# Performance work log

Measured on AMD Instinct MI355X. Metric: run time of the kernel, lower is better.

## Reference

```python
import jax, jax.numpy as jnp
import numpy as np

BS, N, H = 8, 64, 512
L = 5
HH, WW = 14, 14


def setup_inputs() -> dict:
    key = jax.random.key(0)
    ks = jax.random.split(key, 6)
    roi_feature_single = jax.random.normal(ks[0], (BS, N, H), dtype=jnp.float32)
    img_featmap = jax.random.normal(ks[1], (BS, H, HH, WW), dtype=jnp.float32)
    # torch init: weight ~ N(0, 0.01), bias = 0
    node_W = jax.random.normal(ks[2], (L, H, H), dtype=jnp.float32) * 0.01
    node_b = jnp.zeros((L, H), dtype=jnp.float32)
    edge_W = jax.random.normal(ks[3], (L, H, H), dtype=jnp.float32) * 0.01
    edge_b = jnp.zeros((L, H), dtype=jnp.float32)
    full_mask = jax.random.randint(ks[4], (BS, N, N), 0, 2, dtype=jnp.int32)
    return {
        "roi_feature_single": roi_feature_single,
        "img_featmap": img_featmap,
        "node_W": node_W,
        "node_b": node_b,
        "edge_W": edge_W,
        "edge_b": edge_b,
        "full_mask": full_mask,
    }


def reference(roi_feature_single, img_featmap, node_W, node_b, edge_W, edge_b, full_mask):
    # mask: [bs, N, N, 1], float
    mask = full_mask.astype(jnp.float32)[..., None]
    denom = jnp.sum(mask, axis=-2) + 1.0  # [bs, N, 1]

    # AdaptiveAvgPool2d((1,1)) on N*N repeats of img_featmap == global mean over (H, W)
    edge_init = jnp.mean(img_featmap, axis=(2, 3))  # [bs, hidden]
    edge_state = jnp.broadcast_to(edge_init[:, None, None, :], (BS, N, N, H))

    node_state = roi_feature_single  # [bs, N, hidden]

    for t in range(L):
        nm = jnp.einsum('bnh,oh->bno', node_state, node_W[t]) + node_b[t]          # node_fc
        em = jnp.einsum('bijh,oh->bijo', edge_state, edge_W[t]) + edge_b[t]        # edge_fc
        col = nm[:, None, :, :]                      # feature_col_large [bs,1,N,h]
        edge_feat = nm[:, :, None, :] + col + em     # row + col + edge messages
        edge_state = jax.nn.leaky_relu(edge_feat)    # negative_slope=0.01 (torch default)
        agg = jnp.sum(edge_state * col * mask, axis=-2)   # masked sum over j -> [bs,N,h]
        node_feat = (nm + agg) / denom
        node_state = node_state + jax.nn.leaky_relu(node_feat)

    roi_col = jnp.broadcast_to(node_state[:, :, None, :], (BS, N, N, H))
    roi_row = jnp.broadcast_to(node_state[:, None, :, :], (BS, N, N, H))
    return jnp.concatenate([roi_col, roi_row], axis=-1)  # [bs, N, N, 2*hidden]
```

## Files before the change

kernel.cpp:

```cpp
#include <hip/hip_runtime.h>
#include <hip/hip_bf16.h>

#define BS 8
#define NN 64
#define HD 512
#define NLAYER 5

typedef short bf16x8 __attribute__((ext_vector_type(8)));
typedef float f32x4 __attribute__((ext_vector_type(4)));

__device__ __forceinline__ float lrelu(float x) { return x > 0.f ? x : 0.01f * x; }

__device__ __forceinline__ void cp16(const void* g, void* l) {
    __builtin_amdgcn_global_load_lds(
        (const __attribute__((address_space(1))) unsigned int*)g,
        (__attribute__((address_space(3))) unsigned int*)l,
        16, 0, 0);
}

__global__ __launch_bounds__(256) void prep_kernel(
    const float* __restrict__ roi, const float* __restrict__ img,
    const float* __restrict__ nW, const float* __restrict__ eW,
    const int* __restrict__ mask,
    __hip_bfloat16* __restrict__ nWb, __hip_bfloat16* __restrict__ eWb,
    float* __restrict__ nodef, __hip_bfloat16* __restrict__ nodeb,
    float* __restrict__ edge_init, float* __restrict__ denom)
{
    int bid = blockIdx.x, tid = threadIdx.x;
    if (bid < 2560) {
        const float* src = (bid < 1280) ? nW : eW;
        __hip_bfloat16* dst = (bid < 1280) ? nWb : eWb;
        int base = ((bid < 1280) ? bid : bid - 1280) * 1024 + tid * 4;
#pragma unroll
        for (int k = 0; k < 4; ++k) dst[base + k] = __float2bfloat16(src[base + k]);
    } else if (bid < 2816) {
        int base = (bid - 2560) * 1024 + tid * 4;
#pragma unroll
        for (int k = 0; k < 4; ++k) {
            float v = roi[base + k];
            nodef[base + k] = v;
            nodeb[base + k] = __float2bfloat16(v);
        }
    } else if (bid < 3840) {
        int pid = (bid - 2816) * 4 + (tid >> 6);
        int l = tid & 63;
        const float* p = img + (size_t)pid * 196;
        float s = 0.f;
        for (int x = l; x < 196; x += 64) s += p[x];
#pragma unroll
        for (int off = 1; off < 64; off <<= 1) s += __shfl_xor(s, off, 64);
        if (l == 0) edge_init[pid] = s * (1.f / 196.f);
    } else {
        int pid = (bid - 3840) * 256 + tid;
        if (pid < 512) {
            const int* m = mask + pid * 64;
            int s = 0;
#pragma unroll
            for (int j = 0; j < 64; ++j) s += m[j];
            denom[pid] = (float)s + 1.f;
        }
    }
}

__global__ __launch_bounds__(256) void em0_kernel(
    const float* __restrict__ edge_init,
    const float* __restrict__ eW0,
    const float* __restrict__ eB0,
    float* __restrict__ em0)
{
    int W = blockIdx.x * 4 + (threadIdx.x >> 6);
    int l = threadIdx.x & 63;
    int b = W >> 9, o = W & 511;
    const float4* ei = (const float4*)(edge_init + b * 512);
    const float4* w4 = (const float4*)(eW0 + (size_t)o * 512);
    float4 a0 = ei[l * 2], a1 = ei[l * 2 + 1];
    float4 b0 = w4[l * 2], b1 = w4[l * 2 + 1];
    float s = a0.x * b0.x + a0.y * b0.y + a0.z * b0.z + a0.w * b0.w
            + a1.x * b1.x + a1.y * b1.y + a1.z * b1.z + a1.w * b1.w;
#pragma unroll
    for (int off = 1; off < 64; off <<= 1) s += __shfl_xor(s, off, 64);
    if (l == 0) em0[W] = s + eB0[o];
}

__global__ __launch_bounds__(256) void nm_gemm(
    const __hip_bfloat16* __restrict__ A,
    const __hip_bfloat16* __restrict__ W,
    const float* __restrict__ bias,
    float* __restrict__ nm)
{
    __shared__ __align__(16) __hip_bfloat16 sA[64 * 32];
    __shared__ __align__(16) __hip_bfloat16 sB[64 * 32];
    int tid = threadIdx.x;
    int bm = blockIdx.x, bn = blockIdx.y;
    int w = tid >> 6, l = tid & 63;
    int lq = l >> 4, lr = l & 15;

    const char* aBase = (const char*)A + (size_t)bm * 64 * 1024;
    const char* bBase = (const char*)W + (size_t)bn * 64 * 1024;
    int offG = (tid >> 2) * 1024 + (tid & 3) * 16;
    int offL = tid * 16;

    f32x4 acc[4] = {};

    for (int kt = 0; kt < 16; ++kt) {
        int ko = kt * 64;
        cp16(aBase + offG + ko, (char*)sA + offL);
        cp16(bBase + offG + ko, (char*)sB + offL);
        __syncthreads();
        bf16x8 af = *(const bf16x8*)&sA[(w * 16 + lr) * 32 + lq * 8];
#pragma unroll
        for (int ni = 0; ni < 4; ++ni) {
            bf16x8 bfv = *(const bf16x8*)&sB[(ni * 16 + lr) * 32 + lq * 8];
            acc[ni] = __builtin_amdgcn_mfma_f32_16x16x32_bf16(af, bfv, acc[ni], 0, 0, 0);
        }
        __syncthreads();
    }
#pragma unroll
    for (int ni = 0; ni < 4; ++ni) {
        int col = bn * 64 + ni * 16 + lr;
        float bv = bias[col];
#pragma unroll
        for (int r = 0; r < 4; ++r) {
            int row = bm * 64 + w * 16 + lq * 4 + r;
            nm[(size_t)row * 512 + col] = acc[ni][r] + bv;
        }
    }
}

__global__ __launch_bounds__(256) void edge_rank1(
    const float* __restrict__ nm, const float* __restrict__ em0,
    const int* __restrict__ mask,
    __hip_bfloat16* __restrict__ es_dst,
    const float* __restrict__ denom,
    float* __restrict__ nodef, __hip_bfloat16* __restrict__ nodeb)
{
    int g = blockIdx.x >> 1, ch = blockIdx.x & 1;
    int w = threadIdx.x >> 6, l = threadIdx.x & 63;
    int c = ch * 256 + w * 64 + l;
    int b = g >> 6;
    float nmi = nm[(size_t)g * 512 + c];
    float emb = em0[b * 512 + c];
    const float* nmb = nm + (size_t)b * 64 * 512;
    const int* mrow = mask + g * 64;
    __hip_bfloat16* erow = es_dst + (size_t)g * 64 * 512 + c;
    float aggv = 0.f;
#pragma unroll 4
    for (int j = 0; j < 64; ++j) {
        float nmj = nmb[j * 512 + c];
        float es = lrelu(nmi + nmj + emb);
        erow[(size_t)j * 512] = __float2bfloat16(es);
        aggv += es * nmj * (float)mrow[j];
    }
    float nf = (nmi + aggv) / denom[g];
    size_t idx = (size_t)g * 512 + c;
    float ns = nodef[idx] + lrelu(nf);
    nodef[idx] = ns;
    nodeb[idx] = __float2bfloat16(ns);
}

__global__ __launch_bounds__(256) void edge_fused(
    const __hip_bfloat16* __restrict__ es_src,
    const __hip_bfloat16* __restrict__ eW,
    const float* __restrict__ eB,
    const float* __restrict__ nm,
    const int* __restrict__ mask,
    __hip_bfloat16* __restrict__ es_dst,
    const float* __restrict__ denom,
    float* __restrict__ nodef, __hip_bfloat16* __restrict__ nodeb,
    int write_es)
{
    __shared__ __align__(16) __hip_bfloat16 sA[128 * 64];
    __shared__ __align__(16) __hip_bfloat16 sB[128 * 64];
    int tid = threadIdx.x;
    int bn = blockIdx.x, bm = blockIdx.y;
    int w = tid >> 6, l = tid & 63;
    int wm = w >> 1, wn = w & 1;
    int lq = l >> 4, lr = l & 15;

    const char* aBase = (const char*)es_src + (size_t)bm * 128 * 1024;
    const char* bBase = (const char*)eW + (size_t)bn * 128 * 1024;
    int gOff = (tid >> 3) * 1024 + (tid & 7) * 16;
    int lOff = tid * 16;

    f32x4 acc[4][4] = {};

    for (int kt = 0; kt < 8; ++kt) {
        int ko = kt * 128;
#pragma unroll
        for (int i = 0; i < 4; ++i) {
            cp16(aBase + gOff + i * 32768 + ko, (char*)sA + lOff + i * 4096);
            cp16(bBase + gOff + i * 32768 + ko, (char*)sB + lOff + i * 4096);
        }
        __syncthreads();
#pragma unroll
        for (int kk = 0; kk < 2; ++kk) {
            bf16x8 af[4], bfv[4];
#pragma unroll
            for (int mi = 0; mi < 4; ++mi)
                af[mi] = *(const bf16x8*)&sA[(wm * 64 + mi * 16 + lr) * 64 + kk * 32 + lq * 8];
#pragma unroll
            for (int ni = 0; ni < 4; ++ni)
                bfv[ni] = *(const bf16x8*)&sB[(wn * 64 + ni * 16 + lr) * 64 + kk * 32 + lq * 8];
#pragma unroll
            for (int mi = 0; mi < 4; ++mi)
#pragma unroll
                for (int ni = 0; ni < 4; ++ni)
                    acc[mi][ni] = __builtin_amdgcn_mfma_f32_16x16x32_bf16(af[mi], bfv[ni], acc[mi][ni], 0, 0, 0);
        }
        __syncthreads();
    }

    int g = bm * 2 + wm;
    int b = g >> 6;
    int cbase = bn * 128 + wn * 64;

    float nmraw[4], nmi[4];
#pragma unroll
    for (int ni = 0; ni < 4; ++ni) {
        int c = cbase + ni * 16 + lr;
        nmraw[ni] = nm[(size_t)g * 512 + c];
        nmi[ni] = nmraw[ni] + eB[c];
    }
    const float* nmb = nm + (size_t)b * 64 * 512;
    const int* mrow = mask + g * 64;
    float aggv[4] = {0.f, 0.f, 0.f, 0.f};

#pragma unroll
    for (int mi = 0; mi < 4; ++mi) {
#pragma unroll
        for (int r = 0; r < 4; ++r) {
            int j = mi * 16 + lq * 4 + r;
            float mf = (float)mrow[j];
            const float* nrow = nmb + (size_t)j * 512;
            size_t erow = ((size_t)(g * 64 + j)) * 512;
#pragma unroll
            for (int ni = 0; ni < 4; ++ni) {
                int c = cbase + ni * 16 + lr;
                float nmj = nrow[c];
                float es = lrelu(acc[mi][ni][r] + nmi[ni] + nmj);
                if (write_es) es_dst[erow + c] = __float2bfloat16(es);
                aggv[ni] += es * nmj * mf;
            }
        }
    }
    float dinv = denom[g];
#pragma unroll
    for (int ni = 0; ni < 4; ++ni) {
        float v = aggv[ni];
        v += __shfl_xor(v, 16, 64);
        v += __shfl_xor(v, 32, 64);
        if (lq == 0) {
            size_t idx = (size_t)g * 512 + cbase + ni * 16 + lr;
            float nf = (nmraw[ni] + v) / dinv;
            float ns = nodef[idx] + lrelu(nf);
            nodef[idx] = ns;
            nodeb[idx] = __float2bfloat16(ns);
        }
    }
}

__global__ __launch_bounds__(256) void out_kernel(
    const float* __restrict__ nodef, float* __restrict__ out)
{
    size_t ch = (size_t)blockIdx.x * 256 + threadIdx.x;
    int c4 = (int)(ch & 255);
    size_t r = ch >> 8;
    int b = (int)(r >> 12);
    int i = (int)((r >> 6) & 63);
    int j = (int)(r & 63);
    int c = c4 * 4;
    const float* src = (c < 512) ? (nodef + ((size_t)(b * 64 + i)) * 512 + c)
                                 : (nodef + ((size_t)(b * 64 + j)) * 512 + (c - 512));
    *reinterpret_cast<float4*>(out + ch * 4) = *reinterpret_cast<const float4*>(src);
}

extern "C" void kernel_launch(void* const* d_in, const int* in_sizes, int n_in,
                              void* d_out, int out_size, void* d_ws, size_t ws_size,
                              hipStream_t stream) {
    const float* roi  = (const float*)d_in[0];
    const float* img  = (const float*)d_in[1];
    const float* nW   = (const float*)d_in[2];
    const float* nB   = (const float*)d_in[3];
    const float* eW   = (const float*)d_in[4];
    const float* eB   = (const float*)d_in[5];
    const int*   mask = (const int*)d_in[6];

    char* ob = (char*)d_out;
    const size_t ES_BYTES = (size_t)32768 * 512 * 2;
    __hip_bfloat16* es0   = (__hip_bfloat16*)(ob);
    __hip_bfloat16* es1   = (__hip_bfloat16*)(ob + ES_BYTES);
    __hip_bfloat16* eWb   = (__hip_bfloat16*)(ob + 2 * ES_BYTES);
    __hip_bfloat16* nWb   = (__hip_bfloat16*)(ob + 2 * ES_BYTES + 2621440);
    __hip_bfloat16* nodeb = (__hip_bfloat16*)(ob + 2 * ES_BYTES + 5242880);
    float*          nm    = (float*)(ob + 2 * ES_BYTES + 5767168);
    float*       edge_init= (float*)(ob + 2 * ES_BYTES + 6815744);
    float*          em0   = (float*)(ob + 2 * ES_BYTES + 6832128);

    char* ws = (char*)d_ws;
    float* nodef = (float*)(ws);
    float* denom = (float*)(ws + 1048576);
    float* outp  = (float*)d_out;

    prep_kernel<<<3842, 256, 0, stream>>>(roi, img, nW, eW, mask,
                                          nWb, eWb, nodef, nodeb, edge_init, denom);
    em0_kernel<<<1024, 256, 0, stream>>>(edge_init, eW, eB, em0);

    nm_gemm<<<dim3(8, 8), 256, 0, stream>>>(nodeb, nWb, nB, nm);
    edge_rank1<<<1024, 256, 0, stream>>>(nm, em0, mask, es0, denom, nodef, nodeb);

    for (int t = 1; t < NLAYER; ++t) {
        const __hip_bfloat16* src = (t & 1) ? es0 : es1;
        __hip_bfloat16* dst       = (t & 1) ? es1 : es0;
        nm_gemm<<<dim3(8, 8), 256, 0, stream>>>(nodeb, nWb + (size_t)t * 262144,
                                                nB + t * 512, nm);
        edge_fused<<<dim3(4, 256), 256, 0, stream>>>(src, eWb + (size_t)t * 262144,
                                                     eB + t * 512, nm, mask,
                                                     dst, denom, nodef, nodeb,
                                                     (t < 4) ? 1 : 0);
    }

    out_kernel<<<32768, 256, 0, stream>>>(nodef, outp);
}
```

Measured before the change: 425.4 us.

## Fuse next-layer node GEMV into edge kernels and retile edge GEMM per node

Removes the separate nm_gemm launches by computing the next layer's node_fc as a per-row GEMV at the end of each edge kernel, using the freshly updated node state held in shared memory, with ping-pong nm buffers. The edge GEMM is retiled so that one block owns one node row (64 edges × all 512 outputs), which makes that fusion possible; the full weight slice is streamed from L2 by every block. The em0 matvec is merged with the first node GEMM, and the prep conversions are vectorized. The trade-off is more weight traffic per block, a serial fp32 GEMV tail and grids of only 512 blocks, in exchange for fewer launches and dependencies.

```diff
diff --git a/kernel.cpp b/kernel.cpp
--- a/kernel.cpp
+++ b/kernel.cpp
@@ -1,21 +1,24 @@
 #include <hip/hip_runtime.h>
 #include <hip/hip_bf16.h>
 
-#define BS 8
-#define NN 64
-#define HD 512
-#define NLAYER 5
 
 typedef short bf16x8 __attribute__((ext_vector_type(8)));
 typedef float f32x4 __attribute__((ext_vector_type(4)));
 
 __device__ __forceinline__ float lrelu(float x) { return x > 0.f ? x : 0.01f * x; }
+__device__ __forceinline__ float asf(unsigned int u) { return __uint_as_float(u); }
 
 __device__ __forceinline__ void cp16(const void* g, void* l) {
     __builtin_amdgcn_global_load_lds(
         (const __attribute__((address_space(1))) unsigned int*)g,
         (__attribute__((address_space(3))) unsigned int*)l,
         16, 0, 0);
+}
+
+__device__ __forceinline__ void cvt4store(__hip_bfloat16* dst, float4 v) {
+    __hip_bfloat16 tmp[4] = {__float2bfloat16(v.x), __float2bfloat16(v.y),
+                             __float2bfloat16(v.z), __float2bfloat16(v.w)};
+    *(uint2*)dst = *(const uint2*)tmp;
 }
 
 __global__ __launch_bounds__(256) void prep_kernel(
@@ -30,17 +33,13 @@
     if (bid < 2560) {
         const float* src = (bid < 1280) ? nW : eW;
         __hip_bfloat16* dst = (bid < 1280) ? nWb : eWb;
-        int base = ((bid < 1280) ? bid : bid - 1280) * 1024 + tid * 4;
-#pragma unroll
-        for (int k = 0; k < 4; ++k) dst[base + k] = __float2bfloat16(src[base + k]);
+        int i = ((bid < 1280) ? bid : bid - 1280) * 256 + tid;
+        cvt4store(dst + (size_t)i * 4, ((const float4*)src)[i]);
     } else if (bid < 2816) {
-        int base = (bid - 2560) * 1024 + tid * 4;
-#pragma unroll
-        for (int k = 0; k < 4; ++k) {
-            float v = roi[base + k];
-            nodef[base + k] = v;
-            nodeb[base + k] = __float2bfloat16(v);
-        }
+        int i = (bid - 2560) * 256 + tid;
+        float4 v = ((const float4*)roi)[i];
+        ((float4*)nodef)[i] = v;
+        cvt4store(nodeb + (size_t)i * 4, v);
     } else if (bid < 3840) {
         int pid = (bid - 2816) * 4 + (tid >> 6);
         int l = tid & 63;
@@ -48,7 +47,7 @@
         float s = 0.f;
         for (int x = l; x < 196; x += 64) s += p[x];
 #pragma unroll
-        for (int off = 1; off < 64; off <<= 1) s += __shfl_xor(s, off, 64);
+        for (int o = 1; o < 64; o <<= 1) s += __shfl_xor(s, o, 64);
         if (l == 0) edge_init[pid] = s * (1.f / 196.f);
     } else {
         int pid = (bid - 3840) * 256 + tid;
@@ -62,68 +61,86 @@
     }
 }
 
-__global__ __launch_bounds__(256) void em0_kernel(
-    const float* __restrict__ edge_init,
-    const float* __restrict__ eW0,
-    const float* __restrict__ eB0,
-    float* __restrict__ em0)
-{
-    int W = blockIdx.x * 4 + (threadIdx.x >> 6);
-    int l = threadIdx.x & 63;
-    int b = W >> 9, o = W & 511;
-    const float4* ei = (const float4*)(edge_init + b * 512);
-    const float4* w4 = (const float4*)(eW0 + (size_t)o * 512);
-    float4 a0 = ei[l * 2], a1 = ei[l * 2 + 1];
-    float4 b0 = w4[l * 2], b1 = w4[l * 2 + 1];
-    float s = a0.x * b0.x + a0.y * b0.y + a0.z * b0.z + a0.w * b0.w
-            + a1.x * b1.x + a1.y * b1.y + a1.z * b1.z + a1.w * b1.w;
-#pragma unroll
-    for (int off = 1; off < 64; off <<= 1) s += __shfl_xor(s, off, 64);
-    if (l == 0) em0[W] = s + eB0[o];
-}
-
-__global__ __launch_bounds__(256) void nm_gemm(
+__global__ __launch_bounds__(256) void nm0em0_kernel(
     const __hip_bfloat16* __restrict__ A,
-    const __hip_bfloat16* __restrict__ W,
-    const float* __restrict__ bias,
-    float* __restrict__ nm)
+    const __hip_bfloat16* __restrict__ W0,
+    const float* __restrict__ nB,
+    const float* __restrict__ edge_init, const float* __restrict__ eW,
+    const float* __restrict__ eB,
+    float* __restrict__ nm, float* __restrict__ em0)
 {
     __shared__ __align__(16) __hip_bfloat16 sA[64 * 32];
     __shared__ __align__(16) __hip_bfloat16 sB[64 * 32];
-    int tid = threadIdx.x;
-    int bm = blockIdx.x, bn = blockIdx.y;
-    int w = tid >> 6, l = tid & 63;
-    int lq = l >> 4, lr = l & 15;
-
-    const char* aBase = (const char*)A + (size_t)bm * 64 * 1024;
-    const char* bBase = (const char*)W + (size_t)bn * 64 * 1024;
-    int offG = (tid >> 2) * 1024 + (tid & 3) * 16;
-    int offL = tid * 16;
-
-    f32x4 acc[4] = {};
-
-    for (int kt = 0; kt < 16; ++kt) {
-        int ko = kt * 64;
-        cp16(aBase + offG + ko, (char*)sA + offL);
-        cp16(bBase + offG + ko, (char*)sB + offL);
-        __syncthreads();
-        bf16x8 af = *(const bf16x8*)&sA[(w * 16 + lr) * 32 + lq * 8];
+    int blk = blockIdx.x, tid = threadIdx.x;
+    int w = tid >> 6, l = tid & 63, lq = l >> 4, lr = l & 15;
+
+    if (blk < 64) {
+        int bm = blk >> 3, bn = blk & 7;
+        const char* aB = (const char*)A + (size_t)bm * 65536;
+        const char* bB = (const char*)W0 + (size_t)bn * 65536;
+        int offG = (tid >> 2) * 1024 + (tid & 3) * 16;
+        f32x4 acc[4] = {};
+        for (int kt = 0; kt < 16; ++kt) {
+            cp16(aB + offG + kt * 64, (char*)sA + tid * 16);
+            cp16(bB + offG + kt * 64, (char*)sB + tid * 16);
+            __syncthreads();
+            bf16x8 af = *(const bf16x8*)&sA[(w * 16 + lr) * 32 + lq * 8];
+#pragma unroll
+            for (int ni = 0; ni < 4; ++ni) {
+                bf16x8 bv = *(const bf16x8*)&sB[(ni * 16 + lr) * 32 + lq * 8];
+                acc[ni] = __builtin_amdgcn_mfma_f32_16x16x32_bf16(af, bv, acc[ni], 0, 0, 0);
+            }
+            __syncthreads();
+        }
 #pragma unroll
         for (int ni = 0; ni < 4; ++ni) {
-            bf16x8 bfv = *(const bf16x8*)&sB[(ni * 16 + lr) * 32 + lq * 8];
-            acc[ni] = __builtin_amdgcn_mfma_f32_16x16x32_bf16(af, bfv, acc[ni], 0, 0, 0);
-        }
-        __syncthreads();
-    }
-#pragma unroll
-    for (int ni = 0; ni < 4; ++ni) {
-        int col = bn * 64 + ni * 16 + lr;
-        float bv = bias[col];
-#pragma unroll
-        for (int r = 0; r < 4; ++r) {
-            int row = bm * 64 + w * 16 + lq * 4 + r;
-            nm[(size_t)row * 512 + col] = acc[ni][r] + bv;
-        }
+            int col = bn * 64 + ni * 16 + lr;
+            float bv = nB[col];
+#pragma unroll
+            for (int r = 0; r < 4; ++r) {
+                int row = bm * 64 + w * 16 + lq * 4 + r;
+                nm[(size_t)row * 512 + col] = acc[ni][r] + bv;
+            }
+        }
+    } else {
+        int wid = (blk - 64) * 4 + w;
+#pragma unroll
+        for (int k = 0; k < 8; ++k) {
+            int d = wid * 8 + k;
+            int b = d >> 9, o = d & 511;
+            const float4* ei = (const float4*)(edge_init + b * 512);
+            const float4* wv = (const float4*)(eW + (size_t)o * 512);
+            float4 a0 = ei[l * 2], a1 = ei[l * 2 + 1];
+            float4 b0 = wv[l * 2], b1 = wv[l * 2 + 1];
+            float s = a0.x * b0.x + a0.y * b0.y + a0.z * b0.z + a0.w * b0.w
+                    + a1.x * b1.x + a1.y * b1.y + a1.z * b1.z + a1.w * b1.w;
+#pragma unroll
+            for (int o2 = 1; o2 < 64; o2 <<= 1) s += __shfl_xor(s, o2, 64);
+            if (l == 0) em0[d] = s + eB[o];
+        }
+    }
+}
+
+__device__ __forceinline__ void gemv_next(
+    const float* snode, const __hip_bfloat16* __restrict__ Wn,
+    const float* __restrict__ bn, float* __restrict__ nm_out, int g, int tid)
+{
+    const float4* nr4 = (const float4*)snode;
+#pragma unroll
+    for (int oo = 0; oo < 2; ++oo) {
+        int o = tid + oo * 256;
+        const bf16x8* wr = (const bf16x8*)(Wn + (size_t)o * 512);
+        float s = 0.f;
+#pragma unroll 8
+        for (int k = 0; k < 64; ++k) {
+            union { bf16x8 v; uint4 u; } W; W.v = wr[k];
+            float4 n0 = nr4[2 * k], n1 = nr4[2 * k + 1];
+            s += asf(W.u.x << 16) * n0.x + asf(W.u.x & 0xFFFF0000u) * n0.y;
+            s += asf(W.u.y << 16) * n0.z + asf(W.u.y & 0xFFFF0000u) * n0.w;
+            s += asf(W.u.z << 16) * n1.x + asf(W.u.z & 0xFFFF0000u) * n1.y;
+            s += asf(W.u.w << 16) * n1.z + asf(W.u.w & 0xFFFF0000u) * n1.w;
+        }
+        nm_out[(size_t)g * 512 + o] = s + bn[o];
     }
 }
 
@@ -131,100 +148,98 @@
     const float* __restrict__ nm, const float* __restrict__ em0,
     const int* __restrict__ mask,
     __hip_bfloat16* __restrict__ es_dst,
-    const float* __restrict__ denom,
-    float* __restrict__ nodef, __hip_bfloat16* __restrict__ nodeb)
-{
-    int g = blockIdx.x >> 1, ch = blockIdx.x & 1;
-    int w = threadIdx.x >> 6, l = threadIdx.x & 63;
-    int c = ch * 256 + w * 64 + l;
-    int b = g >> 6;
-    float nmi = nm[(size_t)g * 512 + c];
-    float emb = em0[b * 512 + c];
-    const float* nmb = nm + (size_t)b * 64 * 512;
+    const float* __restrict__ denom, float* __restrict__ nodef,
+    const __hip_bfloat16* __restrict__ Wn, const float* __restrict__ bn,
+    float* __restrict__ nm_out)
+{
+    __shared__ float snode[512];
+    int g = blockIdx.x, tid = threadIdx.x, b = g >> 6;
+    const float* nmb = nm + (size_t)b * 32768;
     const int* mrow = mask + g * 64;
-    __hip_bfloat16* erow = es_dst + (size_t)g * 64 * 512 + c;
-    float aggv = 0.f;
+    float dv = denom[g];
+#pragma unroll
+    for (int cc = tid; cc < 512; cc += 256) {
+        float nmi = nm[(size_t)g * 512 + cc];
+        float emb = em0[b * 512 + cc];
+        __hip_bfloat16* erow = es_dst + (size_t)(g * 64) * 512 + cc;
+        float aggv = 0.f;
 #pragma unroll 4
-    for (int j = 0; j < 64; ++j) {
-        float nmj = nmb[j * 512 + c];
-        float es = lrelu(nmi + nmj + emb);
-        erow[(size_t)j * 512] = __float2bfloat16(es);
-        aggv += es * nmj * (float)mrow[j];
-    }
-    float nf = (nmi + aggv) / denom[g];
-    size_t idx = (size_t)g * 512 + c;
-    float ns = nodef[idx] + lrelu(nf);
-    nodef[idx] = ns;
-    nodeb[idx] = __float2bfloat16(ns);
-}
-
-__global__ __launch_bounds__(256) void edge_fused(
+        for (int j = 0; j < 64; ++j) {
+            float nmj = nmb[j * 512 + cc];
+            float es = lrelu(nmi + nmj + emb);
+            erow[(size_t)j * 512] = __float2bfloat16(es);
+            aggv += es * nmj * (float)mrow[j];
+        }
+        float nf = (nmi + aggv) / dv;
+        size_t idx = (size_t)g * 512 + cc;
+        float ns = nodef[idx] + lrelu(nf);
+        nodef[idx] = ns;
+        snode[cc] = ns;
+    }
+    __syncthreads();
+    gemv_next(snode, Wn, bn, nm_out, g, tid);
+}
+
+__global__ void __launch_bounds__(256, 2) edge_kernel(
     const __hip_bfloat16* __restrict__ es_src,
-    const __hip_bfloat16* __restrict__ eW,
-    const float* __restrict__ eB,
-    const float* __restrict__ nm,
+    const __hip_bfloat16* __restrict__ eWt,
+    const float* __restrict__ eBt,
+    const float* __restrict__ nm_in,
     const int* __restrict__ mask,
     __hip_bfloat16* __restrict__ es_dst,
-    const float* __restrict__ denom,
-    float* __restrict__ nodef, __hip_bfloat16* __restrict__ nodeb,
-    int write_es)
-{
-    __shared__ __align__(16) __hip_bfloat16 sA[128 * 64];
-    __shared__ __align__(16) __hip_bfloat16 sB[128 * 64];
-    int tid = threadIdx.x;
-    int bn = blockIdx.x, bm = blockIdx.y;
-    int w = tid >> 6, l = tid & 63;
-    int wm = w >> 1, wn = w & 1;
-    int lq = l >> 4, lr = l & 15;
-
-    const char* aBase = (const char*)es_src + (size_t)bm * 128 * 1024;
-    const char* bBase = (const char*)eW + (size_t)bn * 128 * 1024;
-    int gOff = (tid >> 3) * 1024 + (tid & 7) * 16;
-    int lOff = tid * 16;
-
-    f32x4 acc[4][4] = {};
-
-    for (int kt = 0; kt < 8; ++kt) {
-        int ko = kt * 128;
-#pragma unroll
-        for (int i = 0; i < 4; ++i) {
-            cp16(aBase + gOff + i * 32768 + ko, (char*)sA + lOff + i * 4096);
-            cp16(bBase + gOff + i * 32768 + ko, (char*)sB + lOff + i * 4096);
-        }
+    const float* __restrict__ denom, float* __restrict__ nodef,
+    const __hip_bfloat16* __restrict__ Wn, const float* __restrict__ bn,
+    float* __restrict__ nm_out,
+    int write_es, int do_gemv)
+{
+    __shared__ __align__(16) __hip_bfloat16 sh[18432];
+    __hip_bfloat16* sA = sh;
+    __hip_bfloat16* sB = sh + 2048;
+
+    int g = blockIdx.x, tid = threadIdx.x;
+    int w = tid >> 6, l = tid & 63, lq = l >> 4, lr = l & 15;
+    int b = g >> 6;
+
+    const char* aB = (const char*)es_src + (size_t)g * 65536;
+    const char* bB = (const char*)eWt;
+    int aOff = (tid >> 2) * 1024 + (tid & 3) * 16;
+
+    f32x4 acc[4][8] = {};
+    for (int kt = 0; kt < 16; ++kt) {
+        int ko = kt * 64;
+        cp16(aB + aOff + ko, (char*)sA + tid * 16);
+#pragma unroll
+        for (int i = 0; i < 8; ++i)
+            cp16(bB + aOff + i * 65536 + ko, (char*)sB + tid * 16 + i * 4096);
         __syncthreads();
-#pragma unroll
-        for (int kk = 0; kk < 2; ++kk) {
-            bf16x8 af[4], bfv[4];
-#pragma unroll
-            for (int mi = 0; mi < 4; ++mi)
-                af[mi] = *(const bf16x8*)&sA[(wm * 64 + mi * 16 + lr) * 64 + kk * 32 + lq * 8];
-#pragma unroll
-            for (int ni = 0; ni < 4; ++ni)
-                bfv[ni] = *(const bf16x8*)&sB[(wn * 64 + ni * 16 + lr) * 64 + kk * 32 + lq * 8];
-#pragma unroll
-            for (int mi = 0; mi < 4; ++mi)
-#pragma unroll
-                for (int ni = 0; ni < 4; ++ni)
-                    acc[mi][ni] = __builtin_amdgcn_mfma_f32_16x16x32_bf16(af[mi], bfv[ni], acc[mi][ni], 0, 0, 0);
-        }
+        bf16x8 af[4], bv[8];
+#pragma unroll
+        for (int mi = 0; mi < 4; ++mi)
+            af[mi] = *(const bf16x8*)&sA[(mi * 16 + lr) * 32 + lq * 8];
+#pragma unroll
+        for (int ni = 0; ni < 8; ++ni)
+            bv[ni] = *(const bf16x8*)&sB[(w * 128 + ni * 16 + lr) * 32 + lq * 8];
+#pragma unroll
+        for (int mi = 0; mi < 4; ++mi)
+#pragma unroll
+            for (int ni = 0; ni < 8; ++ni)
+                acc[mi][ni] = __builtin_amdgcn_mfma_f32_16x16x32_bf16(af[mi], bv[ni], acc[mi][ni], 0, 0, 0);
         __syncthreads();
     }
 
-    int g = bm * 2 + wm;
-    int b = g >> 6;
-    int cbase = bn * 128 + wn * 64;
-
-    float nmraw[4], nmi[4];
-#pragma unroll
-    for (int ni = 0; ni < 4; ++ni) {
+    int cbase = w * 128;
+    const float* nmb = nm_in + (size_t)b * 32768;
+    const int* mrow = mask + g * 64;
+    float dv = denom[g];
+
+    float nmraw[8], nmi8[8];
+#pragma unroll
+    for (int ni = 0; ni < 8; ++ni) {
         int c = cbase + ni * 16 + lr;
-        nmraw[ni] = nm[(size_t)g * 512 + c];
-        nmi[ni] = nmraw[ni] + eB[c];
-    }
-    const float* nmb = nm + (size_t)b * 64 * 512;
-    const int* mrow = mask + g * 64;
-    float aggv[4] = {0.f, 0.f, 0.f, 0.f};
-
+        nmraw[ni] = nm_in[(size_t)g * 512 + c];
+        nmi8[ni] = nmraw[ni] + eBt[c];
+    }
+    float aggv[8] = {};
 #pragma unroll
     for (int mi = 0; mi < 4; ++mi) {
 #pragma unroll
@@ -234,28 +249,33 @@
             const float* nrow = nmb + (size_t)j * 512;
             size_t erow = ((size_t)(g * 64 + j)) * 512;
 #pragma unroll
-            for (int ni = 0; ni < 4; ++ni) {
+            for (int ni = 0; ni < 8; ++ni) {
                 int c = cbase + ni * 16 + lr;
                 float nmj = nrow[c];
-                float es = lrelu(acc[mi][ni][r] + nmi[ni] + nmj);
+                float es = lrelu(acc[mi][ni][r] + nmi8[ni] + nmj);
                 if (write_es) es_dst[erow + c] = __float2bfloat16(es);
                 aggv[ni] += es * nmj * mf;
             }
         }
     }
-    float dinv = denom[g];
-#pragma unroll
-    for (int ni = 0; ni < 4; ++ni) {
+    float* snode = (float*)sh;
+#pragma unroll
+    for (int ni = 0; ni < 8; ++ni) {
         float v = aggv[ni];
         v += __shfl_xor(v, 16, 64);
         v += __shfl_xor(v, 32, 64);
         if (lq == 0) {
-            size_t idx = (size_t)g * 512 + cbase + ni * 16 + lr;
-            float nf = (nmraw[ni] + v) / dinv;
+            int c = cbase + ni * 16 + lr;
+            size_t idx = (size_t)g * 512 + c;
+            float nf = (nmraw[ni] + v) / dv;
             float ns = nodef[idx] + lrelu(nf);
             nodef[idx] = ns;
-            nodeb[idx] = __float2bfloat16(ns);
-        }
+            snode[c] = ns;
+        }
+    }
+    if (do_gemv) {
+        __syncthreads();
+        gemv_next(snode, Wn, bn, nm_out, g, tid);
     }
 }
 
@@ -271,7 +291,7 @@
     int c = c4 * 4;
     const float* src = (c < 512) ? (nodef + ((size_t)(b * 64 + i)) * 512 + c)
                                  : (nodef + ((size_t)(b * 64 + j)) * 512 + (c - 512));
-    *reinterpret_cast<float4*>(out + ch * 4) = *reinterpret_cast<const float4*>(src);
+    ((float4*)out)[ch] = *(const float4*)src;
 }
 
 extern "C" void kernel_launch(void* const* d_in, const int* in_sizes, int n_in,
@@ -286,15 +306,15 @@
     const int*   mask = (const int*)d_in[6];
 
     char* ob = (char*)d_out;
-    const size_t ES_BYTES = (size_t)32768 * 512 * 2;
     __hip_bfloat16* es0   = (__hip_bfloat16*)(ob);
-    __hip_bfloat16* es1   = (__hip_bfloat16*)(ob + ES_BYTES);
-    __hip_bfloat16* eWb   = (__hip_bfloat16*)(ob + 2 * ES_BYTES);
-    __hip_bfloat16* nWb   = (__hip_bfloat16*)(ob + 2 * ES_BYTES + 2621440);
-    __hip_bfloat16* nodeb = (__hip_bfloat16*)(ob + 2 * ES_BYTES + 5242880);
-    float*          nm    = (float*)(ob + 2 * ES_BYTES + 5767168);
-    float*       edge_init= (float*)(ob + 2 * ES_BYTES + 6815744);
-    float*          em0   = (float*)(ob + 2 * ES_BYTES + 6832128);
+    __hip_bfloat16* es1   = (__hip_bfloat16*)(ob + 33554432);
+    __hip_bfloat16* eWb   = (__hip_bfloat16*)(ob + 67108864);
+    __hip_bfloat16* nWb   = (__hip_bfloat16*)(ob + 69730304);
+    __hip_bfloat16* nodeb = (__hip_bfloat16*)(ob + 72351744);
+    float*          nmA   = (float*)(ob + 72876032);
+    float*          nmB   = (float*)(ob + 73924608);
+    float*          em0   = (float*)(ob + 74973184);
+    float*       edge_init= (float*)(ob + 74989568);
 
     char* ws = (char*)d_ws;
     float* nodef = (float*)(ws);
@@ -303,21 +323,22 @@
 
     prep_kernel<<<3842, 256, 0, stream>>>(roi, img, nW, eW, mask,
                                           nWb, eWb, nodef, nodeb, edge_init, denom);
-    em0_kernel<<<1024, 256, 0, stream>>>(edge_init, eW, eB, em0);
-
-    nm_gemm<<<dim3(8, 8), 256, 0, stream>>>(nodeb, nWb, nB, nm);
-    edge_rank1<<<1024, 256, 0, stream>>>(nm, em0, mask, es0, denom, nodef, nodeb);
-
-    for (int t = 1; t < NLAYER; ++t) {
+    nm0em0_kernel<<<192, 256, 0, stream>>>(nodeb, nWb, nB, edge_init, eW, eB,
+                                           nmA, em0);
+    edge_rank1<<<512, 256, 0, stream>>>(nmA, em0, mask, es0, denom, nodef,
+                                        nWb + 262144, nB + 512, nmB);
+    for (int t = 1; t < 5; ++t) {
         const __hip_bfloat16* src = (t & 1) ? es0 : es1;
         __hip_bfloat16* dst       = (t & 1) ? es1 : es0;
-        nm_gemm<<<dim3(8, 8), 256, 0, stream>>>(nodeb, nWb + (size_t)t * 262144,
-                                                nB + t * 512, nm);
-        edge_fused<<<dim3(4, 256), 256, 0, stream>>>(src, eWb + (size_t)t * 262144,
-                                                     eB + t * 512, nm, mask,
-                                                     dst, denom, nodef, nodeb,
-                                                     (t < 4) ? 1 : 0);
-    }
-
+        float* nin  = (t & 1) ? nmB : nmA;
+        float* nout = (t & 1) ? nmA : nmB;
+        int tn = (t < 4) ? (t + 1) : t;
+        edge_kernel<<<512, 256, 0, stream>>>(src, eWb + (size_t)t * 262144,
+                                             eB + t * 512, nin, mask, dst,
+                                             denom, nodef,
+                                             nWb + (size_t)tn * 262144,
+                                             nB + tn * 512, nout,
+                                             (t < 4) ? 1 : 0, (t < 4) ? 1 : 0);
+    }
     out_kernel<<<32768, 256, 0, stream>>>(nodef, outp);
 }
```

Result: slower. 547.7 us (+28.8%).
